# Kernel tuning notes

Measured on AMD Instinct MI355X. Metric: run time of the kernel, lower is better.

The kernel has to match this reference:

```python
import jax, jax.numpy as jnp
import numpy as np

NUM_HEADS = 12

def setup_inputs() -> dict:
    key = jax.random.key(0)
    k1, k2, k3 = jax.random.split(key, 3)
    B, H, W, C = 8, 32, 32, 768
    x = jax.random.normal(k1, (B, H, W, C), dtype=jnp.float32)
    qkv_w = jax.random.normal(k2, (3 * C, C), dtype=jnp.float32) * (C ** -0.5)
    qkv_b = jnp.zeros((3 * C,), dtype=jnp.float32)
    proj_w = jax.random.normal(k3, (C, C), dtype=jnp.float32) * (C ** -0.5)
    proj_b = jnp.zeros((C,), dtype=jnp.float32)
    return {"x": x, "qkv_w": qkv_w, "qkv_b": qkv_b, "proj_w": proj_w, "proj_b": proj_b}

def reference(x, qkv_w, qkv_b, proj_w, proj_b):
    B, H, W, C = x.shape
    N = H * W
    h = NUM_HEADS
    d = C // h
    scale = d ** -0.5
    xf = x.reshape(B, N, C)
    # fused QKV projection: [B,N,3C] -> [3,B,h,N,d]
    qkv = (xf @ qkv_w.T + qkv_b).reshape(B, N, 3, h, d).transpose(2, 0, 3, 1, 4)
    q, k, v = qkv[0], qkv[1], qkv[2]  # rope = Identity
    # scaled dot-product attention
    scores = jnp.einsum('bhnd,bhmd->bhnm', q, k) * scale
    attn = jax.nn.softmax(scores, axis=-1)
    out = jnp.einsum('bhnm,bhmd->bhnd', attn, v)
    out = out.transpose(0, 2, 1, 3).reshape(B, N, C)
    out = out @ proj_w.T + proj_b
    return out.reshape(B, H, W, C)
```

## Files before the change

### kernel.cpp

```cpp
#include <hip/hip_runtime.h>
#include <math.h>

#define AS1 __attribute__((address_space(1)))
#define AS3 __attribute__((address_space(3)))

typedef __attribute__((ext_vector_type(8))) short bf16x8;
typedef __attribute__((ext_vector_type(4))) float f32x4;

__device__ __forceinline__ unsigned short f2bf(float f) {
    union { float f; unsigned int i; } v; v.f = f;
    unsigned int r = v.i + 0x7FFFu + ((v.i >> 16) & 1u);
    return (unsigned short)(r >> 16);
}

__device__ __forceinline__ unsigned int pack2bf(float lo, float hi) {
    union { float f; unsigned int i; } a, b; a.f = lo; b.f = hi;
    return __builtin_amdgcn_perm(b.i + 0x8000u, a.i + 0x8000u, 0x07060302u);
}

#define NTOK 1024
#define CCH  768
#define HD   64
#define QKS  1536

#define N1C (8192 * 768 / 4)
#define N2C (2304 * 768 / 4)
#define N3C (768 * 768 / 4)

__global__ void cvt_all(const float* __restrict__ x, const float* __restrict__ w1,
                        const float* __restrict__ w2,
                        unsigned short* __restrict__ xb, unsigned short* __restrict__ w1b,
                        unsigned short* __restrict__ w2b)
{
    int i = blockIdx.x * blockDim.x + threadIdx.x;
    const float4* s; ushort4* d; int k;
    if (i < N1C)            { s = (const float4*)x;  d = (ushort4*)xb;  k = i; }
    else if (i < N1C + N2C) { s = (const float4*)w1; d = (ushort4*)w1b; k = i - N1C; }
    else if (i < N1C + N2C + N3C) { s = (const float4*)w2; d = (ushort4*)w2b; k = i - N1C - N2C; }
    else return;
    const float4 v = s[k];
    ushort4 o;
    o.x = f2bf(v.x); o.y = f2bf(v.y); o.z = f2bf(v.z); o.w = f2bf(v.w);
    d[k] = o;
}

#define PROJ_STAGE(t, buf) do {                                                              \
    __builtin_amdgcn_global_load_lds((AS1 void*)(Ag  + (t) * 32), (AS3 void*)(Asx[buf] + dstA),  16, 0, 0); \
    __builtin_amdgcn_global_load_lds((AS1 void*)(Wg0 + (t) * 32), (AS3 void*)(Bsx[buf] + dstB0), 16, 0, 0); \
    __builtin_amdgcn_global_load_lds((AS1 void*)(Wg1 + (t) * 32), (AS3 void*)(Bsx[buf] + dstB1), 16, 0, 0); \
  } while (0)

#define PROJ_STEP(cur) do {                                                                  \
    bf16x8 af[2], bfv[4];                                                                    \
    _Pragma("unroll")                                                                        \
    for (int i = 0; i < 2; ++i)                                                              \
        af[i] = *(const bf16x8*)((const char*)&Asx[0][0] + (cur) * 4096 + dA + i * 1024);    \
    _Pragma("unroll")                                                                        \
    for (int j = 0; j < 4; ++j)                                                              \
        bfv[j] = *(const bf16x8*)((const char*)&Bsx[0][0] + (cur) * 8192 + dB + j * 1024);   \
    __builtin_amdgcn_s_setprio(1);                                                           \
    _Pragma("unroll")                                                                        \
    for (int i = 0; i < 2; ++i)                                                              \
      _Pragma("unroll")                                                                      \
      for (int j = 0; j < 4; ++j)                                                            \
        acc[i][j] = __builtin_amdgcn_mfma_f32_16x16x32_bf16(af[i], bfv[j], acc[i][j], 0, 0, 0); \
    __builtin_amdgcn_s_setprio(0);                                                           \
  } while (0)

__global__ __launch_bounds__(256, 4)
void gemm_proj(const unsigned short* __restrict__ A,
               const unsigned short* __restrict__ W,
               const float* __restrict__ bias,
               float* __restrict__ Cmat)
{
    const int N = 768, K = 768;
    __shared__ __align__(16) unsigned short Asx[3][64 * 32];
    __shared__ __align__(16) unsigned short Bsx[3][128 * 32];

    const int tid  = threadIdx.x;
    const int wave = tid >> 6;
    const int lane = tid & 63;
    const int quad = lane >> 4;
    const int l15  = lane & 15;
    const int wr   = wave >> 1;
    const int wc   = wave & 1;

    const int lin = blockIdx.x;
    const int idx = (lin & 7) * 96 + (lin >> 3);
    const int mt  = idx / 6;
    const int nt  = idx % 6;
    const int m0  = mt * 64;
    const int n0  = nt * 128;

    const int r  = tid >> 2;
    const int sp = tid & 3;
    const int sl = sp ^ ((r >> 1) & 3);
    const unsigned short* Ag  = A + (size_t)(m0 + r)      * K + sl * 8;
    const unsigned short* Wg0 = W + (size_t)(n0 + r)      * K + sl * 8;
    const unsigned short* Wg1 = W + (size_t)(n0 + 64 + r) * K + sl * 8;
    const int dstA  = tid * 8;
    const int dstB0 = tid * 8;
    const int dstB1 = tid * 8 + 2048;

    int dA = (wr * 32 + l15) * 64 + quad * 16;
    dA ^= ((dA >> 7) & 1) << 4;  dA ^= ((dA >> 8) & 1) << 5;
    int dB = (wc * 64 + l15) * 64 + quad * 16;
    dB ^= ((dB >> 7) & 1) << 4;  dB ^= ((dB >> 8) & 1) << 5;

    f32x4 acc[2][4];
#pragma unroll
    for (int i = 0; i < 2; ++i)
#pragma unroll
        for (int j = 0; j < 4; ++j) acc[i][j] = (f32x4){0.f, 0.f, 0.f, 0.f};

    PROJ_STAGE(0, 0);
    PROJ_STAGE(1, 1);
    asm volatile("s_waitcnt vmcnt(3)" ::: "memory");
    __builtin_amdgcn_s_barrier();
    __builtin_amdgcn_sched_barrier(0);

#pragma unroll
    for (int t = 0; t < 22; ++t) {
        const int cur = t % 3;
        PROJ_STAGE(t + 2, (t + 2) % 3);
        __builtin_amdgcn_sched_barrier(0);
        PROJ_STEP(cur);
        asm volatile("s_waitcnt vmcnt(3)" ::: "memory");
        __builtin_amdgcn_s_barrier();
        __builtin_amdgcn_sched_barrier(0);
    }
    PROJ_STEP(1);
    asm volatile("s_waitcnt vmcnt(0)" ::: "memory");
    __builtin_amdgcn_s_barrier();
    __builtin_amdgcn_sched_barrier(0);
    PROJ_STEP(2);

#pragma unroll
    for (int i = 0; i < 2; ++i) {
        const int row = m0 + wr * 32 + i * 16 + quad * 4;
#pragma unroll
        for (int j = 0; j < 4; ++j) {
            const int col = n0 + wc * 64 + j * 16 + l15;
            const float bv = bias[col];
#pragma unroll
            for (int r2 = 0; r2 < 4; ++r2)
                Cmat[(size_t)(row + r2) * N + col] = acc[i][j][r2] + bv;
        }
    }
}

#define QKV_STAGE(t, buf) do {                                                               \
    __builtin_amdgcn_global_load_lds((AS1 void*)(Ag0 + (t) * 32), (AS3 void*)(As[buf] + dst0), 16, 0, 0); \
    __builtin_amdgcn_global_load_lds((AS1 void*)(Ag1 + (t) * 32), (AS3 void*)(As[buf] + dst1), 16, 0, 0); \
    __builtin_amdgcn_global_load_lds((AS1 void*)(Wg0 + (t) * 32), (AS3 void*)(Bs[buf] + dstB), 16, 0, 0); \
  } while (0)

#define QKV_STEP(cur) do {                                                                   \
    bf16x8 af[4], bfv[4];                                                                    \
    _Pragma("unroll")                                                                        \
    for (int i = 0; i < 4; ++i)                                                              \
        af[i] = *(const bf16x8*)((const char*)&As[0][0] + (cur) * 16384 + dA + i * 1024);    \
    _Pragma("unroll")                                                                        \
    for (int j = 0; j < 4; ++j)                                                              \
        bfv[j] = *(const bf16x8*)((const char*)&Bs[0][0] + (cur) * 8192 + dB + j * 1024);    \
    __builtin_amdgcn_s_setprio(1);                                                           \
    _Pragma("unroll")                                                                        \
    for (int i = 0; i < 4; ++i)                                                              \
      _Pragma("unroll")                                                                      \
      for (int j = 0; j < 4; ++j)                                                            \
        acc[i][j] = __builtin_amdgcn_mfma_f32_16x16x32_bf16(af[i], bfv[j], acc[i][j], 0, 0, 0); \
    __builtin_amdgcn_s_setprio(0);                                                           \
  } while (0)

__global__ __launch_bounds__(512, 4)
void gemm_qkv(const unsigned short* __restrict__ A,
              const unsigned short* __restrict__ W,
              const float* __restrict__ bias,
              unsigned short* __restrict__ qk,
              unsigned short* __restrict__ vT)
{
    const int K = 768;
    __shared__ __align__(16) unsigned short As[3][256 * 32];
    __shared__ __align__(16) unsigned short Bs[3][128 * 32];

    const int tid  = threadIdx.x;
    const int wave = tid >> 6;
    const int lane = tid & 63;
    const int quad = lane >> 4;
    const int l15  = lane & 15;
    const int wr   = wave >> 1;
    const int wc   = wave & 1;

    const int lin = blockIdx.x;
    const int xcd = lin & 7;
    const int j9  = lin >> 3;
    const int bx  = (xcd & 3) * 8 + (j9 & 7);
    const int by  = (xcd >> 2) * 9 + (j9 >> 3);
    const int m0  = bx * 256;
    const int n0  = by * 128;

    const int srow  = tid >> 2;
    const int scolb = ((tid & 3) << 4)
                    ^ (((tid >> 3) & 1) << 4)
                    ^ (((tid >> 4) & 1) << 5);
    const unsigned short* Ag0 = A + (size_t)(m0 + srow)       * K + (scolb >> 1);
    const unsigned short* Ag1 = A + (size_t)(m0 + 128 + srow) * K + (scolb >> 1);
    const unsigned short* Wg0 = W + (size_t)(n0 + srow)       * K + (scolb >> 1);
    const int dst0 = tid * 8;
    const int dst1 = tid * 8 + 4096;
    const int dstB = tid * 8;

    int dA = (wr * 64 + l15) * 64 + quad * 16;
    dA ^= ((dA >> 7) & 1) << 4;  dA ^= ((dA >> 8) & 1) << 5;
    int dB = (wc * 64 + l15) * 64 + quad * 16;
    dB ^= ((dB >> 7) & 1) << 4;  dB ^= ((dB >> 8) & 1) << 5;

    f32x4 acc[4][4];
#pragma unroll
    for (int i = 0; i < 4; ++i)
#pragma unroll
        for (int j = 0; j < 4; ++j) acc[i][j] = (f32x4){0.f, 0.f, 0.f, 0.f};

    QKV_STAGE(0, 0);
    QKV_STAGE(1, 1);
    asm volatile("s_waitcnt vmcnt(3)" ::: "memory");
    __builtin_amdgcn_s_barrier();
    __builtin_amdgcn_sched_barrier(0);

#pragma unroll
    for (int t = 0; t < 22; ++t) {
        const int cur = t % 3;
        QKV_STAGE(t + 2, (t + 2) % 3);
        __builtin_amdgcn_sched_barrier(0);
        QKV_STEP(cur);
        asm volatile("s_waitcnt vmcnt(3)" ::: "memory");
        __builtin_amdgcn_s_barrier();
        __builtin_amdgcn_sched_barrier(0);
    }
    QKV_STEP(1);
    asm volatile("s_waitcnt vmcnt(0)" ::: "memory");
    __builtin_amdgcn_s_barrier();
    __builtin_amdgcn_sched_barrier(0);
    QKV_STEP(2);

    const int colbase = n0 + wc * 64;
    if (colbase < 1536) {
        const float s = (colbase < 768) ? 0.125f : 1.f;
#pragma unroll
        for (int i = 0; i < 4; ++i) {
            const int row = m0 + wr * 64 + i * 16 + quad * 4;
#pragma unroll
            for (int j = 0; j < 4; ++j) {
                const int col = colbase + j * 16 + l15;
                const float bv = bias[col];
#pragma unroll
                for (int r = 0; r < 4; ++r)
                    qk[(size_t)(row + r) * QKS + col] = f2bf((acc[i][j][r] + bv) * s);
            }
        }
    } else {
#pragma unroll
        for (int i = 0; i < 4; ++i) {
            const int m    = m0 + wr * 64 + i * 16 + quad * 4;
            const int b    = m >> 10;
            const int tok  = m & 1023;
            const int tile = tok >> 6;
            const int K0   = tok & 63;
#pragma unroll
            for (int j = 0; j < 4; ++j) {
                const int col = colbase + j * 16 + l15;
                const int c   = col - 1536;
                const int h   = c >> 6, d = c & 63;
                const float bv = bias[col];
                const int bh     = b * 12 + h;
                const int region = (d >> 4) * 2 + (K0 >> 5);
                const int L      = ((K0 >> 3) & 3) * 16 + (d & 15);
                uint2 o;
                o.x = pack2bf(acc[i][j][0] + bv, acc[i][j][1] + bv);
                o.y = pack2bf(acc[i][j][2] + bv, acc[i][j][3] + bv);
                *(uint2*)(vT + (((size_t)(bh * 16 + tile) * 8 + region) << 9) + L * 8 + (K0 & 7)) = o;
            }
        }
    }
}

__global__ __launch_bounds__(256, 4)
void attn_fused(const unsigned short* __restrict__ qk,
                const unsigned short* __restrict__ vT,
                unsigned short* __restrict__ aout)
{
    __shared__ __align__(16) unsigned short Kf[2][8 * 512];
    __shared__ __align__(16) unsigned short Vt[2][8 * 512];
    __shared__ __align__(16) unsigned short Ps[8 * 512];

    const int tid  = threadIdx.x;
    const int wave = tid >> 6;
    const int lane = tid & 63;
    const int quad = lane >> 4;
    const int l15  = lane & 15;

    const int lin = blockIdx.x;
    const int bh  = lin % 96;
    const int qt  = lin / 96;
    const int b   = bh / 12;
    const int h   = bh % 12;

    const unsigned short* Qg  = qk + (size_t)b * NTOK * QKS + (size_t)h * HD;
    const unsigned short* Kg  = Qg + CCH;
    const unsigned short* vTb = vT + (size_t)bh * 16 * 8 * 512;

    const int q0 = qt * 128;

    bf16x8 qf[2][2];
#pragma unroll
    for (int qb = 0; qb < 2; ++qb)
#pragma unroll
        for (int ks = 0; ks < 2; ++ks)
            qf[qb][ks] = *(const bf16x8*)(Qg + (size_t)(q0 + wave * 32 + qb * 16 + l15) * QKS
                                              + ks * 32 + quad * 8);

    f32x4 oacc[2][4];
#pragma unroll
    for (int qb = 0; qb < 2; ++qb)
#pragma unroll
        for (int nb = 0; nb < 4; ++nb) oacc[qb][nb] = (f32x4){0.f, 0.f, 0.f, 0.f};
    float lrow[2] = {0.f, 0.f};

    const unsigned short* kdma = Kg + (size_t)(wave * 16 + l15) * QKS + quad * 8;

#pragma unroll
    for (int ks = 0; ks < 2; ++ks)
        __builtin_amdgcn_global_load_lds((AS1 void*)(kdma + ks * 32),
            (AS3 void*)(Kf[0] + (wave * 2 + ks) * 512 + lane * 8), 16, 0, 0);
#pragma unroll
    for (int u = 0; u < 2; ++u)
        __builtin_amdgcn_global_load_lds((AS1 void*)(vTb + (size_t)(wave * 2 + u) * 512 + lane * 8),
            (AS3 void*)(Vt[0] + (wave * 2 + u) * 512 + lane * 8), 16, 0, 0);

    for (int t = 0; t < 16; ++t) {
        const int cur = t & 1;
        __syncthreads();

        if (t < 15) {
            const int nxt = cur ^ 1;
#pragma unroll
            for (int ks = 0; ks < 2; ++ks)
                __builtin_amdgcn_global_load_lds((AS1 void*)(kdma + (size_t)((t + 1) * 64) * QKS + ks * 32),
                    (AS3 void*)(Kf[nxt] + (wave * 2 + ks) * 512 + lane * 8), 16, 0, 0);
#pragma unroll
            for (int u = 0; u < 2; ++u)
                __builtin_amdgcn_global_load_lds((AS1 void*)(vTb + ((size_t)(t + 1) * 8 + wave * 2 + u) * 512 + lane * 8),
                    (AS3 void*)(Vt[nxt] + (wave * 2 + u) * 512 + lane * 8), 16, 0, 0);
        }

        f32x4 sacc[2][4];
#pragma unroll
        for (int qb = 0; qb < 2; ++qb)
#pragma unroll
            for (int jk = 0; jk < 4; ++jk) sacc[qb][jk] = (f32x4){0.f, 0.f, 0.f, 0.f};
#pragma unroll
        for (int ks = 0; ks < 2; ++ks) {
            bf16x8 kf[4];
#pragma unroll
            for (int jk = 0; jk < 4; ++jk)
                kf[jk] = *(const bf16x8*)(Kf[cur] + (jk * 2 + ks) * 512 + lane * 8);
#pragma unroll
            for (int qb = 0; qb < 2; ++qb)
#pragma unroll
                for (int jk = 0; jk < 4; ++jk)
                    sacc[qb][jk] = __builtin_amdgcn_mfma_f32_16x16x32_bf16(
                        kf[jk], qf[qb][ks], sacc[qb][jk], 0, 0, 0);
        }

#pragma unroll
        for (int qb = 0; qb < 2; ++qb) {
            float rsum = 0.f;
#pragma unroll
            for (int jk = 0; jk < 4; ++jk)
#pragma unroll
                for (int r = 0; r < 4; ++r) {
                    const float p = __expf(sacc[qb][jk][r]);
                    sacc[qb][jk][r] = p;
                    rsum += p;
                }
            rsum += __shfl_xor(rsum, 16);
            rsum += __shfl_xor(rsum, 32);
            lrow[qb] += rsum;
        }

#pragma unroll
        for (int p = 0; p < 2; ++p) {
#pragma unroll
            for (int qb = 0; qb < 2; ++qb)
#pragma unroll
                for (int jh = 0; jh < 2; ++jh) {
                    const int jk = 2 * p + jh;
                    uint2 o;
                    o.x = pack2bf(sacc[qb][jk][0], sacc[qb][jk][1]);
                    o.y = pack2bf(sacc[qb][jk][2], sacc[qb][jk][3]);
                    const int off = (wave * 2 + qb) * 512
                                  + ((jh * 2 + (quad >> 1)) * 16 + l15) * 8 + (quad & 1) * 4;
                    *(uint2*)&Ps[off] = o;
                }
            bf16x8 pf[2], vf[4];
#pragma unroll
            for (int qb = 0; qb < 2; ++qb)
                pf[qb] = *(const bf16x8*)(Ps + (wave * 2 + qb) * 512 + lane * 8);
#pragma unroll
            for (int nb = 0; nb < 4; ++nb)
                vf[nb] = *(const bf16x8*)(Vt[cur] + (nb * 2 + p) * 512 + lane * 8);
#pragma unroll
            for (int qb = 0; qb < 2; ++qb)
#pragma unroll
                for (int nb = 0; nb < 4; ++nb)
                    oacc[qb][nb] = __builtin_amdgcn_mfma_f32_16x16x32_bf16(
                        vf[nb], pf[qb], oacc[qb][nb], 0, 0, 0);
        }
    }

#pragma unroll
    for (int qb = 0; qb < 2; ++qb) {
        const float inv = 1.f / lrow[qb];
        const size_t tok = (size_t)(b * NTOK + q0 + wave * 32 + qb * 16 + l15);
#pragma unroll
        for (int nb = 0; nb < 4; ++nb) {
            uint2 o;
            o.x = pack2bf(oacc[qb][nb][0] * inv, oacc[qb][nb][1] * inv);
            o.y = pack2bf(oacc[qb][nb][2] * inv, oacc[qb][nb][3] * inv);
            *(uint2*)(aout + tok * CCH + h * HD + nb * 16 + quad * 4) = o;
        }
    }
}

extern "C" void kernel_launch(void* const* d_in, const int* in_sizes, int n_in,
                              void* d_out, int out_size, void* d_ws, size_t ws_size,
                              hipStream_t stream)
{
    const float* x      = (const float*)d_in[0];
    const float* qkv_w  = (const float*)d_in[1];
    const float* qkv_b  = (const float*)d_in[2];
    const float* proj_w = (const float*)d_in[3];
    const float* proj_b = (const float*)d_in[4];
    float* out = (float*)d_out;

    unsigned short* qk  = (unsigned short*)d_ws;
    unsigned short* att = qk  + (size_t)8192 * 1536;
    unsigned short* xb  = att + (size_t)8192 * 768;
    unsigned short* wqb = xb  + (size_t)8192 * 768;
    unsigned short* wpb = wqb + (size_t)2304 * 768;
    unsigned short* vT  = wpb + (size_t)768 * 768;

    cvt_all<<<dim3((N1C + N2C + N3C + 255) / 256), dim3(256), 0, stream>>>(x, qkv_w, proj_w, xb, wqb, wpb);
    gemm_qkv<<<dim3(576), dim3(512), 0, stream>>>(xb, wqb, qkv_b, qk, vT);
    attn_fused<<<dim3(768), dim3(256), 0, stream>>>(qk, vT, att);
    gemm_proj<<<dim3(768), dim3(256), 0, stream>>>(att, wpb, proj_b, out);
}
```

Before: 187.7 us.

## Deepen GEMM pipelines to four stages and shrink QKV tiles to 128x128

Both GEMM kernels move from a three-buffer to a four-buffer LDS pipeline, so three K-tiles are in flight, with the vmcnt waits and epilogue adjusted to match. The QKV GEMM also drops from 256x128 tiles with 512 threads to 128x128 tiles with 256 threads and twice as many blocks, remapping blocks across XCDs. The aim is to hide global-load latency better and improve occupancy and load balance. In exchange each block reuses less data and the kernels use more LDS.

```diff
diff --git a/kernel.cpp b/kernel.cpp
--- a/kernel.cpp
+++ b/kernel.cpp
@@ -74,8 +74,8 @@
                float* __restrict__ Cmat)
 {
     const int N = 768, K = 768;
-    __shared__ __align__(16) unsigned short Asx[3][64 * 32];
-    __shared__ __align__(16) unsigned short Bsx[3][128 * 32];
+    __shared__ __align__(16) unsigned short Asx[4][64 * 32];
+    __shared__ __align__(16) unsigned short Bsx[4][128 * 32];
 
     const int tid  = threadIdx.x;
     const int wave = tid >> 6;
@@ -115,25 +115,29 @@
 
     PROJ_STAGE(0, 0);
     PROJ_STAGE(1, 1);
-    asm volatile("s_waitcnt vmcnt(3)" ::: "memory");
-    __builtin_amdgcn_s_barrier();
-    __builtin_amdgcn_sched_barrier(0);
-
-#pragma unroll
-    for (int t = 0; t < 22; ++t) {
-        const int cur = t % 3;
-        PROJ_STAGE(t + 2, (t + 2) % 3);
+    PROJ_STAGE(2, 2);
+    asm volatile("s_waitcnt vmcnt(6)" ::: "memory");
+    __builtin_amdgcn_s_barrier();
+    __builtin_amdgcn_sched_barrier(0);
+
+#pragma unroll
+    for (int t = 0; t < 21; ++t) {
+        PROJ_STAGE(t + 3, (t + 3) & 3);
         __builtin_amdgcn_sched_barrier(0);
-        PROJ_STEP(cur);
-        asm volatile("s_waitcnt vmcnt(3)" ::: "memory");
+        PROJ_STEP(t & 3);
+        asm volatile("s_waitcnt vmcnt(6)" ::: "memory");
         __builtin_amdgcn_s_barrier();
         __builtin_amdgcn_sched_barrier(0);
     }
     PROJ_STEP(1);
+    asm volatile("s_waitcnt vmcnt(3)" ::: "memory");
+    __builtin_amdgcn_s_barrier();
+    __builtin_amdgcn_sched_barrier(0);
+    PROJ_STEP(2);
     asm volatile("s_waitcnt vmcnt(0)" ::: "memory");
     __builtin_amdgcn_s_barrier();
     __builtin_amdgcn_sched_barrier(0);
-    PROJ_STEP(2);
+    PROJ_STEP(3);
 
 #pragma unroll
     for (int i = 0; i < 2; ++i) {
@@ -152,14 +156,15 @@
 #define QKV_STAGE(t, buf) do {                                                               \
     __builtin_amdgcn_global_load_lds((AS1 void*)(Ag0 + (t) * 32), (AS3 void*)(As[buf] + dst0), 16, 0, 0); \
     __builtin_amdgcn_global_load_lds((AS1 void*)(Ag1 + (t) * 32), (AS3 void*)(As[buf] + dst1), 16, 0, 0); \
-    __builtin_amdgcn_global_load_lds((AS1 void*)(Wg0 + (t) * 32), (AS3 void*)(Bs[buf] + dstB), 16, 0, 0); \
+    __builtin_amdgcn_global_load_lds((AS1 void*)(Wg0 + (t) * 32), (AS3 void*)(Bs[buf] + dst0), 16, 0, 0); \
+    __builtin_amdgcn_global_load_lds((AS1 void*)(Wg1 + (t) * 32), (AS3 void*)(Bs[buf] + dst1), 16, 0, 0); \
   } while (0)
 
 #define QKV_STEP(cur) do {                                                                   \
     bf16x8 af[4], bfv[4];                                                                    \
     _Pragma("unroll")                                                                        \
     for (int i = 0; i < 4; ++i)                                                              \
-        af[i] = *(const bf16x8*)((const char*)&As[0][0] + (cur) * 16384 + dA + i * 1024);    \
+        af[i] = *(const bf16x8*)((const char*)&As[0][0] + (cur) * 8192 + dA + i * 1024);     \
     _Pragma("unroll")                                                                        \
     for (int j = 0; j < 4; ++j)                                                              \
         bfv[j] = *(const bf16x8*)((const char*)&Bs[0][0] + (cur) * 8192 + dB + j * 1024);    \
@@ -172,7 +177,7 @@
     __builtin_amdgcn_s_setprio(0);                                                           \
   } while (0)
 
-__global__ __launch_bounds__(512, 4)
+__global__ __launch_bounds__(256, 2)
 void gemm_qkv(const unsigned short* __restrict__ A,
               const unsigned short* __restrict__ W,
               const float* __restrict__ bias,
@@ -180,8 +185,8 @@
               unsigned short* __restrict__ vT)
 {
     const int K = 768;
-    __shared__ __align__(16) unsigned short As[3][256 * 32];
-    __shared__ __align__(16) unsigned short Bs[3][128 * 32];
+    __shared__ __align__(16) unsigned short As[4][128 * 32];
+    __shared__ __align__(16) unsigned short Bs[4][128 * 32];
 
     const int tid  = threadIdx.x;
     const int wave = tid >> 6;
@@ -192,23 +197,22 @@
     const int wc   = wave & 1;
 
     const int lin = blockIdx.x;
-    const int xcd = lin & 7;
-    const int j9  = lin >> 3;
-    const int bx  = (xcd & 3) * 8 + (j9 & 7);
-    const int by  = (xcd >> 2) * 9 + (j9 >> 3);
-    const int m0  = bx * 256;
-    const int n0  = by * 128;
+    const int idx = (lin & 7) * 144 + (lin >> 3);
+    const int mt  = idx / 18;
+    const int nt  = idx % 18;
+    const int m0  = mt * 128;
+    const int n0  = nt * 128;
 
     const int srow  = tid >> 2;
     const int scolb = ((tid & 3) << 4)
                     ^ (((tid >> 3) & 1) << 4)
                     ^ (((tid >> 4) & 1) << 5);
-    const unsigned short* Ag0 = A + (size_t)(m0 + srow)       * K + (scolb >> 1);
-    const unsigned short* Ag1 = A + (size_t)(m0 + 128 + srow) * K + (scolb >> 1);
-    const unsigned short* Wg0 = W + (size_t)(n0 + srow)       * K + (scolb >> 1);
+    const unsigned short* Ag0 = A + (size_t)(m0 + srow)      * K + (scolb >> 1);
+    const unsigned short* Ag1 = A + (size_t)(m0 + 64 + srow) * K + (scolb >> 1);
+    const unsigned short* Wg0 = W + (size_t)(n0 + srow)      * K + (scolb >> 1);
+    const unsigned short* Wg1 = W + (size_t)(n0 + 64 + srow) * K + (scolb >> 1);
     const int dst0 = tid * 8;
-    const int dst1 = tid * 8 + 4096;
-    const int dstB = tid * 8;
+    const int dst1 = tid * 8 + 2048;
 
     int dA = (wr * 64 + l15) * 64 + quad * 16;
     dA ^= ((dA >> 7) & 1) << 4;  dA ^= ((dA >> 8) & 1) << 5;
@@ -223,25 +227,29 @@
 
     QKV_STAGE(0, 0);
     QKV_STAGE(1, 1);
-    asm volatile("s_waitcnt vmcnt(3)" ::: "memory");
-    __builtin_amdgcn_s_barrier();
-    __builtin_amdgcn_sched_barrier(0);
-
-#pragma unroll
-    for (int t = 0; t < 22; ++t) {
-        const int cur = t % 3;
-        QKV_STAGE(t + 2, (t + 2) % 3);
+    QKV_STAGE(2, 2);
+    asm volatile("s_waitcnt vmcnt(8)" ::: "memory");
+    __builtin_amdgcn_s_barrier();
+    __builtin_amdgcn_sched_barrier(0);
+
+#pragma unroll
+    for (int t = 0; t < 21; ++t) {
+        QKV_STAGE(t + 3, (t + 3) & 3);
         __builtin_amdgcn_sched_barrier(0);
-        QKV_STEP(cur);
-        asm volatile("s_waitcnt vmcnt(3)" ::: "memory");
+        QKV_STEP(t & 3);
+        asm volatile("s_waitcnt vmcnt(8)" ::: "memory");
         __builtin_amdgcn_s_barrier();
         __builtin_amdgcn_sched_barrier(0);
     }
     QKV_STEP(1);
+    asm volatile("s_waitcnt vmcnt(4)" ::: "memory");
+    __builtin_amdgcn_s_barrier();
+    __builtin_amdgcn_sched_barrier(0);
+    QKV_STEP(2);
     asm volatile("s_waitcnt vmcnt(0)" ::: "memory");
     __builtin_amdgcn_s_barrier();
     __builtin_amdgcn_sched_barrier(0);
-    QKV_STEP(2);
+    QKV_STEP(3);
 
     const int colbase = n0 + wc * 64;
     if (colbase < 1536) {
@@ -451,7 +459,7 @@
     unsigned short* vT  = wpb + (size_t)768 * 768;
 
     cvt_all<<<dim3((N1C + N2C + N3C + 255) / 256), dim3(256), 0, stream>>>(x, qkv_w, proj_w, xb, wqb, wpb);
-    gemm_qkv<<<dim3(576), dim3(512), 0, stream>>>(xb, wqb, qkv_b, qk, vT);
+    gemm_qkv<<<dim3(1152), dim3(256), 0, stream>>>(xb, wqb, qkv_b, qk, vT);
     attn_fused<<<dim3(768), dim3(256), 0, stream>>>(qk, vT, att);
     gemm_proj<<<dim3(768), dim3(256), 0, stream>>>(att, wpb, proj_b, out);
 }
```

After: 190.5 us. About the same (+1.5%).
